# Optimization experiments

Measured on AMD Instinct MI355X. Metric: run time of the kernel, lower is better.

The kernel has to match this reference:

```python
import jax, jax.numpy as jnp
import numpy as np

N_NODES = 100000


def gcn_conv(x, src, dst, W, b, n):
    """PyG GCNConv: add self-loops, symmetric normalization, out = A_hat @ (x W) + b."""
    loop = jnp.arange(n, dtype=src.dtype)
    s = jnp.concatenate([src, loop])
    d = jnp.concatenate([dst, loop])
    deg = jnp.zeros((n,), dtype=x.dtype).at[d].add(1.0)
    dinv = jnp.where(deg > 0, jax.lax.rsqrt(deg), 0.0)
    norm = dinv[s] * dinv[d]                      # [E+N]
    h = x @ W                                     # [N, out]
    msg = h[s] * norm[:, None]                    # [E+N, out] gather
    out = jax.ops.segment_sum(msg, d, num_segments=n)  # scatter-add
    return out + b


def prelu(x, a):
    return jnp.where(x >= 0, x, a * x)


def setup_inputs() -> dict:
    key = jax.random.key(0)
    ks = jax.random.split(key, 12)
    n, din, dout, dproj = N_NODES, 128, 128, 128
    dhid = 2 * dout
    x = jax.random.normal(ks[0], (n, din), dtype=jnp.float32)
    edge_index = jax.random.randint(ks[1], (2, 1600000), 0, n, dtype=jnp.int64)

    def glorot(k, fan_in, fan_out):
        lim = np.sqrt(6.0 / (fan_in + fan_out))
        return jax.random.uniform(k, (fan_in, fan_out), jnp.float32, -lim, lim)

    return {
        "x": x,
        "edge_index": edge_index,
        "W1": glorot(ks[2], din, dhid),
        "b1": jnp.zeros((dhid,), jnp.float32),
        "W2": glorot(ks[3], dhid, dout),
        "b2": jnp.zeros((dout,), jnp.float32),
        "a": jnp.asarray(0.25, jnp.float32),          # PReLU weight (num_parameters=1)
        "fc1_w": glorot(ks[4], dout, dproj),
        "fc1_b": jnp.zeros((dproj,), jnp.float32),
        "fc2_w": glorot(ks[5], dproj, dout),
        "fc2_b": jnp.zeros((dout,), jnp.float32),
    }


def reference(x, edge_index, W1, b1, W2, b2, a, fc1_w, fc1_b, fc2_w, fc2_b):
    n = x.shape[0]
    src, dst = edge_index[0], edge_index[1]
    out = prelu(gcn_conv(x, src, dst, W1, b1, n), a)
    out = prelu(gcn_conv(out, src, dst, W2, b2, n), a)
    proj = jax.nn.relu(out @ fc1_w + fc1_b)
    proj = proj @ fc2_w + fc2_b
    return (out, proj)
```

## Files before the change

kernel.cpp:

```cpp
#include <hip/hip_runtime.h>


typedef __attribute__((ext_vector_type(4))) float  f32x4;
typedef __attribute__((ext_vector_type(8))) __bf16 bf16x8;
typedef __attribute__((ext_vector_type(8))) short  short8;

__device__ __forceinline__ bf16x8 as_bf(short8 s) {
    union { short8 s; bf16x8 b; } u; u.s = s; return u.b;
}

__device__ __forceinline__ short2 split1(float x) {
    unsigned u = __float_as_uint(x);
    short hi = (short)(u >> 16);
    float hif = __uint_as_float(u & 0xFFFF0000u);
    short lo = (short)(__float_as_uint(x - hif) >> 16);
    return make_short2(hi, lo);
}

__global__ void deg_kernel(const int* __restrict__ dst, int* __restrict__ deg, int E) {
    int e = blockIdx.x * blockDim.x + threadIdx.x;
    if (e < E) atomicAdd(&deg[dst[e]], 1);
}

__global__ __launch_bounds__(256)
void part_kernel(const int* __restrict__ deg, int* __restrict__ bsum,
                 float* __restrict__ dinv, int n) {
    int tid = threadIdx.x;
    int base = blockIdx.x * 1024 + tid * 4;
    int d[4] = {0, 0, 0, 0};
    if (base + 3 < n) {
        int4 v = *(const int4*)(deg + base);
        d[0] = v.x; d[1] = v.y; d[2] = v.z; d[3] = v.w;
    } else {
        for (int j = 0; j < 4; ++j) if (base + j < n) d[j] = deg[base + j];
    }
    for (int j = 0; j < 4; ++j)
        if (base + j < n) dinv[base + j] = rsqrtf((float)(d[j] + 1));
    int s = d[0] + d[1] + d[2] + d[3];
    for (int off = 32; off > 0; off >>= 1) s += __shfl_down(s, off);
    __shared__ int wsum[4];
    if ((tid & 63) == 0) wsum[tid >> 6] = s;
    __syncthreads();
    if (tid == 0) bsum[blockIdx.x] = wsum[0] + wsum[1] + wsum[2] + wsum[3];
}

__global__ __launch_bounds__(1024)
void topscan_kernel(const int* __restrict__ bsum, int* __restrict__ bbase, int nb) {
    __shared__ int sh[1024];
    int tid = threadIdx.x;
    int own = (tid < nb) ? bsum[tid] : 0;
    sh[tid] = own;
    __syncthreads();
    for (int off = 1; off < 1024; off <<= 1) {
        int t = (tid >= off) ? sh[tid - off] : 0;
        __syncthreads();
        sh[tid] += t;
        __syncthreads();
    }
    if (tid < nb) bbase[tid] = sh[tid] - own;
}

__global__ __launch_bounds__(256)
void offs_kernel(const int* __restrict__ deg, const int* __restrict__ bbase,
                 int* __restrict__ offsets, int n) {
    int tid = threadIdx.x;
    int base = blockIdx.x * 1024 + tid * 4;
    int d[4] = {0, 0, 0, 0};
    if (base + 3 < n) {
        int4 v = *(const int4*)(deg + base);
        d[0] = v.x; d[1] = v.y; d[2] = v.z; d[3] = v.w;
    } else {
        for (int j = 0; j < 4; ++j) if (base + j < n) d[j] = deg[base + j];
    }
    int s = d[0] + d[1] + d[2] + d[3];
    __shared__ int sh[256];
    sh[tid] = s;
    __syncthreads();
    for (int off = 1; off < 256; off <<= 1) {
        int t = (tid >= off) ? sh[tid - off] : 0;
        __syncthreads();
        sh[tid] += t;
        __syncthreads();
    }
    int run = bbase[blockIdx.x] + sh[tid] - s;
    for (int j = 0; j < 4; ++j) {
        int idx = base + j;
        if (idx <= n) offsets[idx] = run;
        if (idx < n) run += d[j];
    }
}

__global__ void fill_kernel(const int* __restrict__ src, const int* __restrict__ dst,
                            const int* __restrict__ offsets, int* __restrict__ cursor,
                            int* __restrict__ csr, int E) {
    int e = blockIdx.x * blockDim.x + threadIdx.x;
    if (e < E) {
        int d = dst[e];
        int pos = offsets[d] + atomicAdd(&cursor[d], 1);
        csr[pos] = src[e];
    }
}

__global__ void wconv_kernel(const float* __restrict__ W, short* __restrict__ Wt_hi,
                             short* __restrict__ Wt_lo, int K, int N) {
    int idx = blockIdx.x * blockDim.x + threadIdx.x;
    if (idx >= K * N) return;
    int nn = idx / K, kk = idx - nn * K;
    short2 s = split1(W[(size_t)kk * N + nn]);
    Wt_hi[idx] = s.x;
    Wt_lo[idx] = s.y;
}

__global__ __launch_bounds__(256)
void agg128_kernel(const float* __restrict__ g, const int* __restrict__ csr,
                   const int* __restrict__ offsets, const float* __restrict__ dinv,
                   const float* __restrict__ bias, const float* __restrict__ a_ptr,
                   float* __restrict__ out, int n) {
    int w = threadIdx.x >> 6;
    int lane = threadIdx.x & 63;
    int v = blockIdx.x * 4 + w;
    if (v >= n) return;
    const char* gb = (const char*)g;
    unsigned loff = (unsigned)lane * 8u;
    float dv = dinv[v];
    float2 self = *(const float2*)(gb + ((unsigned)v * 512u + loff));
    float accx = dv * self.x;
    float accy = dv * self.y;
    int e = offsets[v], end = offsets[v + 1];
#pragma unroll 1
    for (; e < end; e += 8) {
        int   idx[8];
        float dd[8];
        float2 mm[8];
#pragma unroll
        for (int j = 0; j < 8; ++j) {
            int ee = e + j;
            idx[j] = csr[ee < end ? ee : end - 1];
        }
#pragma unroll
        for (int j = 0; j < 8; ++j)
            dd[j] = (e + j < end) ? dinv[idx[j]] : 0.f;
#pragma unroll
        for (int j = 0; j < 8; ++j)
            mm[j] = *(const float2*)(gb + ((unsigned)idx[j] * 512u + loff));
#pragma unroll
        for (int j = 0; j < 8; ++j) {
            accx += dd[j] * mm[j].x;
            accy += dd[j] * mm[j].y;
        }
    }
    accx *= dv;
    accy *= dv;
    if (bias) {
        float a = *a_ptr;
        float2 bb = ((const float2*)bias)[lane];
        accx += bb.x;
        accy += bb.y;
        accx = accx >= 0.f ? accx : a * accx;
        accy = accy >= 0.f ? accy : a * accy;
    }
    float2 r; r.x = accx; r.y = accy;
    ((float2*)out)[(size_t)v * 64 + lane] = r;
}

__global__ __launch_bounds__(256)
void gemm_kernel(const float* __restrict__ A, const short* __restrict__ Bt_hi,
                 const short* __restrict__ Bt_lo, float* __restrict__ C,
                 int M, int K, int N,
                 const float* __restrict__ bias, int act,
                 const float* __restrict__ a_ptr) {
    const int tid = threadIdx.x;
    const int wave = tid >> 6, lane = tid & 63;
    const int quad = lane >> 4, l16 = lane & 15;
    const int row0 = blockIdx.x * 64 + wave * 16;
    const int col0 = blockIdx.y * 64;
    const int m = row0 + l16;
    const int mc = m < M ? m : M - 1;
    const float* Arow = A + (size_t)mc * K + quad * 8;

    f32x4 acc[4] = {{0.f, 0.f, 0.f, 0.f}, {0.f, 0.f, 0.f, 0.f},
                    {0.f, 0.f, 0.f, 0.f}, {0.f, 0.f, 0.f, 0.f}};

    for (int k0 = 0; k0 < K; k0 += 32) {
        float4 av0 = *(const float4*)(Arow + k0);
        float4 av1 = *(const float4*)(Arow + k0 + 4);
        short8 ah, al;
        short2 s;
        s = split1(av0.x); ah[0] = s.x; al[0] = s.y;
        s = split1(av0.y); ah[1] = s.x; al[1] = s.y;
        s = split1(av0.z); ah[2] = s.x; al[2] = s.y;
        s = split1(av0.w); ah[3] = s.x; al[3] = s.y;
        s = split1(av1.x); ah[4] = s.x; al[4] = s.y;
        s = split1(av1.y); ah[5] = s.x; al[5] = s.y;
        s = split1(av1.z); ah[6] = s.x; al[6] = s.y;
        s = split1(av1.w); ah[7] = s.x; al[7] = s.y;
        bf16x8 a_hi = as_bf(ah), a_lo = as_bf(al);
#pragma unroll
        for (int t = 0; t < 4; ++t) {
            size_t boff = (size_t)(col0 + t * 16 + l16) * K + k0 + quad * 8;
            bf16x8 b_hi = as_bf(*(const short8*)(Bt_hi + boff));
            bf16x8 b_lo = as_bf(*(const short8*)(Bt_lo + boff));
            acc[t] = __builtin_amdgcn_mfma_f32_16x16x32_bf16(a_hi, b_hi, acc[t], 0, 0, 0);
            acc[t] = __builtin_amdgcn_mfma_f32_16x16x32_bf16(a_hi, b_lo, acc[t], 0, 0, 0);
            acc[t] = __builtin_amdgcn_mfma_f32_16x16x32_bf16(a_lo, b_hi, acc[t], 0, 0, 0);
        }
    }

    float a = (act == 2) ? *a_ptr : 0.f;
#pragma unroll
    for (int t = 0; t < 4; ++t) {
        int col = col0 + t * 16 + l16;
        float bb = bias ? bias[col] : 0.f;
#pragma unroll
        for (int r = 0; r < 4; ++r) {
            int row = row0 + quad * 4 + r;
            if (row < M) {
                float o = acc[t][r] + bb;
                if (act == 1) o = fmaxf(o, 0.f);
                else if (act == 2) o = o >= 0.f ? o : a * o;
                C[(size_t)row * N + col] = o;
            }
        }
    }
}

extern "C" void kernel_launch(void* const* d_in, const int* in_sizes, int n_in,
                              void* d_out, int out_size, void* d_ws, size_t ws_size,
                              hipStream_t stream) {
    const float* x     = (const float*)d_in[0];
    const int*   ei    = (const int*)d_in[1];
    const float* W1    = (const float*)d_in[2];
    const float* b1    = (const float*)d_in[3];
    const float* W2    = (const float*)d_in[4];
    const float* b2    = (const float*)d_in[5];
    const float* a_ptr = (const float*)d_in[6];
    const float* fc1_w = (const float*)d_in[7];
    const float* fc1_b = (const float*)d_in[8];
    const float* fc2_w = (const float*)d_in[9];
    const float* fc2_b = (const float*)d_in[10];

    const int n = in_sizes[0] / 128;
    const int E = in_sizes[1] / 2;
    const int* src = ei;
    const int* dst = ei + E;
    const int nb = (n + 1023) >> 10;

    float* out_final  = (float*)d_out;
    float* proj_final = out_final + (size_t)n * 128;
    float* out1       = (float*)d_out;

    char* p = (char*)d_ws;
    auto take = [&](size_t bytes) -> char* {
        char* q = p;
        p += (bytes + 1023) & ~(size_t)1023;
        return q;
    };
    int*   deg     = (int*)take((size_t)n * 4);
    int*   offsets = (int*)take(((size_t)n + 1) * 4);
    int*   cursor  = (int*)take((size_t)n * 4);
    float* dinv    = (float*)take((size_t)n * 4);
    int*   bsum    = (int*)take((size_t)1024 * 4);
    int*   bbase   = (int*)take((size_t)1024 * 4);
    int*   csr     = (int*)take((size_t)E * 4);
    short* W1t_hi  = (short*)take((size_t)256 * 128 * 2);
    short* W1t_lo  = (short*)take((size_t)256 * 128 * 2);
    short* W2t_hi  = (short*)take((size_t)128 * 256 * 2);
    short* W2t_lo  = (short*)take((size_t)128 * 256 * 2);
    short* f1t_hi  = (short*)take((size_t)128 * 128 * 2);
    short* f1t_lo  = (short*)take((size_t)128 * 128 * 2);
    short* f2t_hi  = (short*)take((size_t)128 * 128 * 2);
    short* f2t_lo  = (short*)take((size_t)128 * 128 * 2);
    float* bufA    = (float*)take((size_t)n * 128 * 4);

    (void)hipMemsetAsync(deg, 0, (size_t)n * 4, stream);
    (void)hipMemsetAsync(cursor, 0, (size_t)n * 4, stream);

    wconv_kernel<<<(128 * 256 + 255) / 256, 256, 0, stream>>>(W1, W1t_hi, W1t_lo, 128, 256);
    wconv_kernel<<<(256 * 128 + 255) / 256, 256, 0, stream>>>(W2, W2t_hi, W2t_lo, 256, 128);
    wconv_kernel<<<(128 * 128 + 255) / 256, 256, 0, stream>>>(fc1_w, f1t_hi, f1t_lo, 128, 128);
    wconv_kernel<<<(128 * 128 + 255) / 256, 256, 0, stream>>>(fc2_w, f2t_hi, f2t_lo, 128, 128);

    deg_kernel<<<(E + 255) / 256, 256, 0, stream>>>(dst, deg, E);
    part_kernel<<<nb, 256, 0, stream>>>(deg, bsum, dinv, n);
    topscan_kernel<<<1, 1024, 0, stream>>>(bsum, bbase, nb);
    offs_kernel<<<nb, 256, 0, stream>>>(deg, bbase, offsets, n);
    fill_kernel<<<(E + 255) / 256, 256, 0, stream>>>(src, dst, offsets, cursor, csr, E);

    const int mblk = (n + 63) / 64;

    agg128_kernel<<<(n + 3) / 4, 256, 0, stream>>>(x, csr, offsets, dinv,
                                                   nullptr, nullptr, bufA, n);
    gemm_kernel<<<dim3(mblk, 4), 256, 0, stream>>>(bufA, W1t_hi, W1t_lo, out1,
                                                   n, 128, 256, b1, 2, a_ptr);

    gemm_kernel<<<dim3(mblk, 2), 256, 0, stream>>>(out1, W2t_hi, W2t_lo, bufA,
                                                   n, 256, 128, nullptr, 0, nullptr);
    agg128_kernel<<<(n + 3) / 4, 256, 0, stream>>>(bufA, csr, offsets, dinv,
                                                   b2, a_ptr, out_final, n);

    gemm_kernel<<<dim3(mblk, 2), 256, 0, stream>>>(out_final, f1t_hi, f1t_lo, bufA,
                                                   n, 128, 128, fc1_b, 1, nullptr);
    gemm_kernel<<<dim3(mblk, 2), 256, 0, stream>>>(bufA, f2t_hi, f2t_lo, proj_final,
                                                   n, 128, 128, fc2_b, 0, nullptr);
}
```

Before: 971.8 us.

## Keep weight fragments in registers and loop blocks over multiple row tiles

The GEMM now preloads the whole 128-deep K slice of the split-bf16 weight fragments into registers once per block, then loops over four 64-row tiles, so weights are no longer reloaded from memory on every k-step. Operands are swapped in the MFMA so each lane holds four consecutive output columns, which allows float4 stores. The K=256 GEMM is split into two K=128 launches, the second accumulating into the output. This cuts B traffic and store instructions, but costs many more registers (lower occupancy), an extra read-modify-write pass over the K=256 output, and one more launch.

```diff
diff --git a/kernel.cpp b/kernel.cpp
--- a/kernel.cpp
+++ b/kernel.cpp
@@ -164,61 +164,93 @@
 }
 
 __global__ __launch_bounds__(256)
-void gemm_kernel(const float* __restrict__ A, const short* __restrict__ Bt_hi,
-                 const short* __restrict__ Bt_lo, float* __restrict__ C,
-                 int M, int K, int N,
-                 const float* __restrict__ bias, int act,
-                 const float* __restrict__ a_ptr) {
-    const int tid = threadIdx.x;
+void gemm64_kernel(const float* __restrict__ A, int lda,
+                   const short* __restrict__ Bt_hi, const short* __restrict__ Bt_lo,
+                   float* __restrict__ C, int M, int N, int k_base,
+                   int mtiles, int tpb,
+                   const float* __restrict__ bias, int act,
+                   const float* __restrict__ a_ptr, int accum) {
+    const int tid  = threadIdx.x;
     const int wave = tid >> 6, lane = tid & 63;
     const int quad = lane >> 4, l16 = lane & 15;
-    const int row0 = blockIdx.x * 64 + wave * 16;
     const int col0 = blockIdx.y * 64;
-    const int m = row0 + l16;
-    const int mc = m < M ? m : M - 1;
-    const float* Arow = A + (size_t)mc * K + quad * 8;
-
-    f32x4 acc[4] = {{0.f, 0.f, 0.f, 0.f}, {0.f, 0.f, 0.f, 0.f},
-                    {0.f, 0.f, 0.f, 0.f}, {0.f, 0.f, 0.f, 0.f}};
-
-    for (int k0 = 0; k0 < K; k0 += 32) {
-        float4 av0 = *(const float4*)(Arow + k0);
-        float4 av1 = *(const float4*)(Arow + k0 + 4);
-        short8 ah, al;
-        short2 s;
-        s = split1(av0.x); ah[0] = s.x; al[0] = s.y;
-        s = split1(av0.y); ah[1] = s.x; al[1] = s.y;
-        s = split1(av0.z); ah[2] = s.x; al[2] = s.y;
-        s = split1(av0.w); ah[3] = s.x; al[3] = s.y;
-        s = split1(av1.x); ah[4] = s.x; al[4] = s.y;
-        s = split1(av1.y); ah[5] = s.x; al[5] = s.y;
-        s = split1(av1.z); ah[6] = s.x; al[6] = s.y;
-        s = split1(av1.w); ah[7] = s.x; al[7] = s.y;
-        bf16x8 a_hi = as_bf(ah), a_lo = as_bf(al);
+
+    bf16x8 bf[4][4][2];
+#pragma unroll
+    for (int kt = 0; kt < 4; ++kt)
 #pragma unroll
         for (int t = 0; t < 4; ++t) {
-            size_t boff = (size_t)(col0 + t * 16 + l16) * K + k0 + quad * 8;
-            bf16x8 b_hi = as_bf(*(const short8*)(Bt_hi + boff));
-            bf16x8 b_lo = as_bf(*(const short8*)(Bt_lo + boff));
-            acc[t] = __builtin_amdgcn_mfma_f32_16x16x32_bf16(a_hi, b_hi, acc[t], 0, 0, 0);
-            acc[t] = __builtin_amdgcn_mfma_f32_16x16x32_bf16(a_hi, b_lo, acc[t], 0, 0, 0);
-            acc[t] = __builtin_amdgcn_mfma_f32_16x16x32_bf16(a_lo, b_hi, acc[t], 0, 0, 0);
-        }
-    }
-
-    float a = (act == 2) ? *a_ptr : 0.f;
-#pragma unroll
-    for (int t = 0; t < 4; ++t) {
-        int col = col0 + t * 16 + l16;
-        float bb = bias ? bias[col] : 0.f;
-#pragma unroll
-        for (int r = 0; r < 4; ++r) {
-            int row = row0 + quad * 4 + r;
-            if (row < M) {
-                float o = acc[t][r] + bb;
-                if (act == 1) o = fmaxf(o, 0.f);
-                else if (act == 2) o = o >= 0.f ? o : a * o;
-                C[(size_t)row * N + col] = o;
+            size_t off = (size_t)(col0 + t * 16 + l16) * lda + k_base + kt * 32 + quad * 8;
+            bf[kt][t][0] = as_bf(*(const short8*)(Bt_hi + off));
+            bf[kt][t][1] = as_bf(*(const short8*)(Bt_lo + off));
+        }
+
+    const float aw = (act == 2) ? *a_ptr : 0.f;
+
+    const int t0 = blockIdx.x * tpb;
+    const int t1 = (t0 + tpb < mtiles) ? t0 + tpb : mtiles;
+    for (int tile = t0; tile < t1; ++tile) {
+        const int m = tile * 64 + wave * 16 + l16;
+        const int mc = m < M ? m : M - 1;
+        const float* Ap = A + (size_t)mc * lda + k_base + quad * 8;
+
+        float4 av[8];
+#pragma unroll
+        for (int kt = 0; kt < 4; ++kt) {
+            av[2 * kt]     = *(const float4*)(Ap + kt * 32);
+            av[2 * kt + 1] = *(const float4*)(Ap + kt * 32 + 4);
+        }
+
+        f32x4 acc[4];
+#pragma unroll
+        for (int t = 0; t < 4; ++t) acc[t] = (f32x4){0.f, 0.f, 0.f, 0.f};
+
+#pragma unroll
+        for (int kt = 0; kt < 4; ++kt) {
+            float4 v0 = av[2 * kt], v1 = av[2 * kt + 1];
+            short8 ah, al;
+            short2 s;
+            s = split1(v0.x); ah[0] = s.x; al[0] = s.y;
+            s = split1(v0.y); ah[1] = s.x; al[1] = s.y;
+            s = split1(v0.z); ah[2] = s.x; al[2] = s.y;
+            s = split1(v0.w); ah[3] = s.x; al[3] = s.y;
+            s = split1(v1.x); ah[4] = s.x; al[4] = s.y;
+            s = split1(v1.y); ah[5] = s.x; al[5] = s.y;
+            s = split1(v1.z); ah[6] = s.x; al[6] = s.y;
+            s = split1(v1.w); ah[7] = s.x; al[7] = s.y;
+            bf16x8 a_hi = as_bf(ah), a_lo = as_bf(al);
+#pragma unroll
+            for (int t = 0; t < 4; ++t) {
+                acc[t] = __builtin_amdgcn_mfma_f32_16x16x32_bf16(bf[kt][t][0], a_hi, acc[t], 0, 0, 0);
+                acc[t] = __builtin_amdgcn_mfma_f32_16x16x32_bf16(bf[kt][t][1], a_hi, acc[t], 0, 0, 0);
+                acc[t] = __builtin_amdgcn_mfma_f32_16x16x32_bf16(bf[kt][t][0], a_lo, acc[t], 0, 0, 0);
+            }
+        }
+
+        if (m < M) {
+            float* Crow = C + (size_t)m * N + col0 + quad * 4;
+#pragma unroll
+            for (int t = 0; t < 4; ++t) {
+                float4 v;
+                v.x = acc[t][0]; v.y = acc[t][1]; v.z = acc[t][2]; v.w = acc[t][3];
+                if (accum) {
+                    float4 o = *(const float4*)(Crow + t * 16);
+                    v.x += o.x; v.y += o.y; v.z += o.z; v.w += o.w;
+                }
+                if (bias) {
+                    float4 bb = *(const float4*)(bias + col0 + t * 16 + quad * 4);
+                    v.x += bb.x; v.y += bb.y; v.z += bb.z; v.w += bb.w;
+                }
+                if (act == 1) {
+                    v.x = fmaxf(v.x, 0.f); v.y = fmaxf(v.y, 0.f);
+                    v.z = fmaxf(v.z, 0.f); v.w = fmaxf(v.w, 0.f);
+                } else if (act == 2) {
+                    v.x = v.x >= 0.f ? v.x : aw * v.x;
+                    v.y = v.y >= 0.f ? v.y : aw * v.y;
+                    v.z = v.z >= 0.f ? v.z : aw * v.z;
+                    v.w = v.w >= 0.f ? v.w : aw * v.w;
+                }
+                *(float4*)(Crow + t * 16) = v;
             }
         }
     }
@@ -286,20 +318,24 @@
     offs_kernel<<<nb, 256, 0, stream>>>(deg, bbase, offsets, n);
     fill_kernel<<<(E + 255) / 256, 256, 0, stream>>>(src, dst, offsets, cursor, csr, E);
 
-    const int mblk = (n + 63) / 64;
+    const int mtiles = (n + 63) / 64;
+    const int TPB = 4;
+    const int gx = (mtiles + TPB - 1) / TPB;
 
     agg128_kernel<<<(n + 3) / 4, 256, 0, stream>>>(x, csr, offsets, dinv,
                                                    nullptr, nullptr, bufA, n);
-    gemm_kernel<<<dim3(mblk, 4), 256, 0, stream>>>(bufA, W1t_hi, W1t_lo, out1,
-                                                   n, 128, 256, b1, 2, a_ptr);
-
-    gemm_kernel<<<dim3(mblk, 2), 256, 0, stream>>>(out1, W2t_hi, W2t_lo, bufA,
-                                                   n, 256, 128, nullptr, 0, nullptr);
+    gemm64_kernel<<<dim3(gx, 4), 256, 0, stream>>>(bufA, 128, W1t_hi, W1t_lo, out1,
+                                                   n, 256, 0, mtiles, TPB, b1, 2, a_ptr, 0);
+
+    gemm64_kernel<<<dim3(gx, 2), 256, 0, stream>>>(out1, 256, W2t_hi, W2t_lo, bufA,
+                                                   n, 128, 0, mtiles, TPB, nullptr, 0, nullptr, 0);
+    gemm64_kernel<<<dim3(gx, 2), 256, 0, stream>>>(out1, 256, W2t_hi, W2t_lo, bufA,
+                                                   n, 128, 128, mtiles, TPB, nullptr, 0, nullptr, 1);
     agg128_kernel<<<(n + 3) / 4, 256, 0, stream>>>(bufA, csr, offsets, dinv,
                                                    b2, a_ptr, out_final, n);
 
-    gemm_kernel<<<dim3(mblk, 2), 256, 0, stream>>>(out_final, f1t_hi, f1t_lo, bufA,
-                                                   n, 128, 128, fc1_b, 1, nullptr);
-    gemm_kernel<<<dim3(mblk, 2), 256, 0, stream>>>(bufA, f2t_hi, f2t_lo, proj_final,
-                                                   n, 128, 128, fc2_b, 0, nullptr);
-}
+    gemm64_kernel<<<dim3(gx, 2), 256, 0, stream>>>(out_final, 128, f1t_hi, f1t_lo, bufA,
+                                                   n, 128, 0, mtiles, TPB, fc1_b, 1, nullptr, 0);
+    gemm64_kernel<<<dim3(gx, 2), 256, 0, stream>>>(bufA, 128, f2t_hi, f2t_lo, proj_final,
+                                                   n, 128, 0, mtiles, TPB, fc2_b, 0, nullptr, 0);
+}
```

Result: faster. 816.2 us (-16.0%).
